# Kernel optimization log

Hardware: AMD Instinct MI355X
Metric: run time of the kernel (lower is better)

Reference implementation:

```python
import jax, jax.numpy as jnp
import numpy as np

N_NODES = 100000
IN_CH = 64
HID = 16
HEADS = 4
OUT_CH = 1
NEG_SLOPE = 0.2
EPS = 1e-16


def gat_conv(x, src, dst, W, att_src, att_dst, bias, heads, out_ch, concat):
    """PyG-style GATConv. src/dst already include self-loops.
    x: [N, F_in]; W: [F_in, heads*out_ch]; att_*: [heads, out_ch]; bias: [heads*out_ch] or [out_ch]."""
    n = x.shape[0]
    h = (x @ W).reshape(n, heads, out_ch)                     # [N,H,C]
    a_src = jnp.einsum('nhc,hc->nh', h, att_src)              # [N,H]
    a_dst = jnp.einsum('nhc,hc->nh', h, att_dst)              # [N,H]
    alpha = jax.nn.leaky_relu(a_src[src] + a_dst[dst], NEG_SLOPE)  # [E,H]
    # segment softmax over incoming edges of each destination node
    m = jax.ops.segment_max(alpha, dst, num_segments=n)       # [N,H]
    e = jnp.exp(alpha - m[dst])
    denom = jax.ops.segment_sum(e, dst, num_segments=n)
    alpha = e / (denom[dst] + EPS)                            # [E,H]
    msg = h[src] * alpha[:, :, None]                          # [E,H,C]
    out = jax.ops.segment_sum(msg, dst, num_segments=n)       # [N,H,C]
    out = out.reshape(n, heads * out_ch) if concat else out.mean(axis=1)
    return out + bias


def setup_inputs() -> dict:
    key = jax.random.key(0)
    ks = jax.random.split(key, 10)
    x = jax.random.normal(ks[0], (N_NODES, IN_CH), dtype=jnp.float32)
    edge_index = jax.random.randint(ks[1], (2, 1600000), 0, N_NODES, dtype=jnp.int64)
    s = 0.1
    W1 = jax.random.normal(ks[2], (IN_CH, HEADS * HID), dtype=jnp.float32) * s
    att_src1 = jax.random.normal(ks[3], (HEADS, HID), dtype=jnp.float32) * s
    att_dst1 = jax.random.normal(ks[4], (HEADS, HID), dtype=jnp.float32) * s
    b1 = jnp.zeros((HEADS * HID,), dtype=jnp.float32)
    W2 = jax.random.normal(ks[5], (HEADS * HID, OUT_CH), dtype=jnp.float32) * s
    att_src2 = jax.random.normal(ks[6], (1, OUT_CH), dtype=jnp.float32) * s
    att_dst2 = jax.random.normal(ks[7], (1, OUT_CH), dtype=jnp.float32) * s
    b2 = jnp.zeros((OUT_CH,), dtype=jnp.float32)
    return {"x": x, "edge_index": edge_index, "W1": W1, "att_src1": att_src1,
            "att_dst1": att_dst1, "b1": b1, "W2": W2, "att_src2": att_src2,
            "att_dst2": att_dst2, "b2": b2}


def reference(x, edge_index, W1, att_src1, att_dst1, b1, W2, att_src2, att_dst2, b2):
    n = x.shape[0]
    loop = jnp.arange(n, dtype=edge_index.dtype)
    src = jnp.concatenate([edge_index[0], loop])  # self-loops (PyG default)
    dst = jnp.concatenate([edge_index[1], loop])
    h = gat_conv(x, src, dst, W1, att_src1, att_dst1, b1, HEADS, HID, concat=True)
    h = jax.nn.elu(h)
    out = gat_conv(h, src, dst, W2, att_src2, att_dst2, b2, 1, OUT_CH, concat=False)
    return out.squeeze()
```

## Files before the change

kernel.cpp:

```cpp
#include <hip/hip_runtime.h>
#include <hip/hip_fp16.h>

#define NN   100000
#define E0   1600000
#define ET   1700000
#define NEG  0.2f
#define EPSV 1e-16f
#define NBK  1563
#define CAP  1536
#define BS   1024
#define NBLK4 ((ET + 4 * BS - 1) / (4 * BS))
#define GEMM_NB 782
#define BC_NB   416

typedef _Float16 half8 __attribute__((ext_vector_type(8)));
typedef float f32x16 __attribute__((ext_vector_type(16)));

__global__ __launch_bounds__(256) void k_g1bc(
    const float* __restrict__ x, const int* __restrict__ ei,
    const float* __restrict__ W1, const float* __restrict__ as1,
    const float* __restrict__ ad1,
    __half* __restrict__ h1h, float* __restrict__ asrc1, float* __restrict__ adst1,
    int* __restrict__ bcnt)
{
    int t = threadIdx.x;
    if (blockIdx.x >= GEMM_NB) {
        __shared__ int cnt[NBK];
        for (int i = t; i < NBK; i += 256) cnt[i] = 0;
        __syncthreads();
        int base = (blockIdx.x - GEMM_NB) * (256 * 16);
#pragma unroll
        for (int k = 0; k < 16; ++k) {
            int idx = base + k * 256 + t;
            if (idx < ET) {
                int d = (idx < E0) ? ei[E0 + idx] : (idx - E0);
                atomicAdd(&cnt[d >> 6], 1);
            }
        }
        __syncthreads();
        for (int i = t; i < NBK; i += 256) if (cnt[i]) atomicAdd(&bcnt[i], cnt[i]);
        return;
    }
    __shared__ float Wl[4096];
    __shared__ float Ul[512];
    for (int i = t; i < 4096; i += 256) Wl[i] = W1[i];
    __syncthreads();
    if (t < 64) {
        int k = t;
#pragma unroll
        for (int h = 0; h < 4; ++h) {
            float su = 0.f, du = 0.f;
#pragma unroll
            for (int c = 0; c < 16; ++c) {
                float w = Wl[k * 64 + h * 16 + c];
                su += w * as1[h * 16 + c];
                du += w * ad1[h * 16 + c];
            }
            Ul[k * 8 + h] = su;
            Ul[k * 8 + 4 + h] = du;
        }
    }
    __syncthreads();
    int lane = t & 63, wv = t >> 6;
    int col = lane & 31, q = lane >> 5;
    half8 bf0[4], bf1[4], bf2[4];
#pragma unroll
    for (int kc = 0; kc < 4; ++kc) {
#pragma unroll
        for (int j = 0; j < 8; ++j) {
            int k = kc * 16 + q * 8 + j;
            bf0[kc][j] = (_Float16)Wl[k * 64 + col];
            bf1[kc][j] = (_Float16)Wl[k * 64 + 32 + col];
            bf2[kc][j] = (col < 8) ? (_Float16)Ul[k * 8 + col] : (_Float16)0.f;
        }
    }
    int tile = blockIdx.x * 4 + wv;
    int n0 = tile * 32;
    if (n0 >= NN) return;
    half8 af[4];
    const float* xrow = x + (size_t)(n0 + col) * 64;
#pragma unroll
    for (int kc = 0; kc < 4; ++kc) {
        float4 xa = *(const float4*)(xrow + kc * 16 + q * 8);
        float4 xb = *(const float4*)(xrow + kc * 16 + q * 8 + 4);
        af[kc][0] = (_Float16)xa.x; af[kc][1] = (_Float16)xa.y;
        af[kc][2] = (_Float16)xa.z; af[kc][3] = (_Float16)xa.w;
        af[kc][4] = (_Float16)xb.x; af[kc][5] = (_Float16)xb.y;
        af[kc][6] = (_Float16)xb.z; af[kc][7] = (_Float16)xb.w;
    }
    f32x16 c0 = {}, c1 = {}, c2 = {};
#pragma unroll
    for (int kc = 0; kc < 4; ++kc) {
        c0 = __builtin_amdgcn_mfma_f32_32x32x16_f16(af[kc], bf0[kc], c0, 0, 0, 0);
        c1 = __builtin_amdgcn_mfma_f32_32x32x16_f16(af[kc], bf1[kc], c1, 0, 0, 0);
        c2 = __builtin_amdgcn_mfma_f32_32x32x16_f16(af[kc], bf2[kc], c2, 0, 0, 0);
    }
#pragma unroll
    for (int reg = 0; reg < 16; ++reg) {
        int row = (reg & 3) + 8 * (reg >> 2) + 4 * q;
        h1h[(size_t)(n0 + row) * 64 + col]      = __float2half(c0[reg]);
        h1h[(size_t)(n0 + row) * 64 + 32 + col] = __float2half(c1[reg]);
    }
    if (col < 8) {
        float* dst = (col < 4) ? asrc1 : adst1;
        int h = col & 3;
#pragma unroll
        for (int reg = 0; reg < 16; ++reg) {
            int row = (reg & 3) + 8 * (reg >> 2) + 4 * q;
            dst[(n0 + row) * 4 + h] = c2[reg];
        }
    }
}

__global__ __launch_bounds__(1024) void k_bscan(const int* __restrict__ bcnt,
                                                int* __restrict__ bbase, int* __restrict__ bcursor)
{
    int t = threadIdx.x;
    int i0 = 2 * t, i1 = 2 * t + 1;
    int a = (i0 < NBK) ? bcnt[i0] : 0;
    int b = (i1 < NBK) ? bcnt[i1] : 0;
    int s = a + b;
    int lane = t & 63, wid = t >> 6;
    int sc = s;
#pragma unroll
    for (int off = 1; off < 64; off <<= 1) {
        int u = __shfl_up(sc, off, 64);
        if (lane >= off) sc += u;
    }
    __shared__ int wsum[16];
    if (lane == 63) wsum[wid] = sc;
    __syncthreads();
    int woff = 0;
    for (int k = 0; k < wid; ++k) woff += wsum[k];
    int excl = sc - s + woff;
    if (i0 < NBK) { bbase[i0] = excl;     bcursor[i0] = excl; }
    if (i1 < NBK) { bbase[i1] = excl + a; bcursor[i1] = excl + a; }
}

__global__ __launch_bounds__(BS) void k_bscat(const int* __restrict__ ei,
                                              int* __restrict__ bcursor, int* __restrict__ bin)
{
    __shared__ int cnt[NBK];
    __shared__ int base[NBK];
    int t = threadIdx.x;
    for (int i = t; i < NBK; i += BS) cnt[i] = 0;
    __syncthreads();
    int blk = blockIdx.x * (BS * 4);
    int b[4], r[4], pk[4];
#pragma unroll
    for (int k = 0; k < 4; ++k) {
        int idx = blk + k * BS + t;
        r[k] = -1;
        if (idx < ET) {
            int s, d;
            if (idx < E0) { s = ei[idx]; d = ei[E0 + idx]; } else { s = d = idx - E0; }
            b[k] = d >> 6;
            pk[k] = s | ((d & 63) << 17);
            r[k] = atomicAdd(&cnt[b[k]], 1);
        }
    }
    __syncthreads();
    for (int i = t; i < NBK; i += BS) if (cnt[i]) base[i] = atomicAdd(&bcursor[i], cnt[i]);
    __syncthreads();
#pragma unroll
    for (int k = 0; k < 4; ++k)
        if (r[k] >= 0) bin[base[b[k]] + r[k]] = pk[k];
}

__global__ __launch_bounds__(256) void k_e1agg(
    const int* __restrict__ bin, const int* __restrict__ bbase, const int* __restrict__ bcnt,
    const float* __restrict__ asrc1, const float* __restrict__ adst1,
    const __half* __restrict__ h1h, const float* __restrict__ b1,
    const float* __restrict__ W2, float* __restrict__ g)
{
    __shared__ int lcsr[CAP];
    __shared__ int deg[64], cur[64];
    int b = blockIdx.x;
    int t = threadIdx.x;
    int beg = bbase[b], cnt = bcnt[b];
    if (cnt > CAP) cnt = CAP;
    if (t < 64) deg[t] = 0;
    __syncthreads();
    for (int i = t; i < cnt; i += 256) atomicAdd(&deg[bin[beg + i] >> 17], 1);
    __syncthreads();
    if (t < 64) {
        int v = deg[t];
        int sc = v;
#pragma unroll
        for (int off = 1; off < 64; off <<= 1) {
            int u = __shfl_up(sc, off, 64);
            if (t >= off) sc += u;
        }
        cur[t] = sc - v;
    }
    __syncthreads();
    for (int i = t; i < cnt; i += 256) {
        int e = bin[beg + i];
        int r = atomicAdd(&cur[e >> 17], 1);
        lcsr[r] = e & 0x1FFFF;
    }
    __syncthreads();
    int hh = t & 3;
    int nl = t >> 2;
    int n = b * 64 + nl;
    if (n >= NN) return;
    int je = cur[nl];
    int jb = je - deg[nl];
    float ad = adst1[n * 4 + hh];
    float acc[16];
#pragma unroll
    for (int c = 0; c < 16; ++c) acc[c] = 0.f;
    float den = 0.f;
    for (int j = jb; j < je; ++j) {
        int s = lcsr[j];
        float as = asrc1[s * 4 + hh];
        float a = as + ad; a = a > 0.f ? a : NEG * a;
        float ev = __expf(a);
        den += ev;
        const uint4* hp = (const uint4*)(h1h + (size_t)s * 64 + hh * 16);
        uint4 r0 = hp[0], r1 = hp[1];
#define U4ACC(r, base) { \
        float2 f0 = __half22float2(*(const __half2*)&r.x); \
        float2 f1 = __half22float2(*(const __half2*)&r.y); \
        float2 f2 = __half22float2(*(const __half2*)&r.z); \
        float2 f3 = __half22float2(*(const __half2*)&r.w); \
        acc[base+0] += ev * f0.x; acc[base+1] += ev * f0.y; \
        acc[base+2] += ev * f1.x; acc[base+3] += ev * f1.y; \
        acc[base+4] += ev * f2.x; acc[base+5] += ev * f2.y; \
        acc[base+6] += ev * f3.x; acc[base+7] += ev * f3.y; }
        U4ACC(r0, 0) U4ACC(r1, 8)
#undef U4ACC
    }
    float inv = 1.f / (den + EPSV);
    const float4* bp = (const float4*)(b1 + hh * 16);
    const float4* wp = (const float4*)(W2 + hh * 16);
    float gv = 0.f;
#pragma unroll
    for (int q = 0; q < 4; ++q) {
        float4 bb = bp[q], w2 = wp[q];
        float v0 = acc[4*q+0] * inv + bb.x; v0 = v0 > 0.f ? v0 : __expf(v0) - 1.f;
        float v1 = acc[4*q+1] * inv + bb.y; v1 = v1 > 0.f ? v1 : __expf(v1) - 1.f;
        float v2 = acc[4*q+2] * inv + bb.z; v2 = v2 > 0.f ? v2 : __expf(v2) - 1.f;
        float v3 = acc[4*q+3] * inv + bb.w; v3 = v3 > 0.f ? v3 : __expf(v3) - 1.f;
        gv += v0 * w2.x + v1 * w2.y + v2 * w2.z + v3 * w2.w;
    }
    gv += __shfl_xor(gv, 1);
    gv += __shfl_xor(gv, 2);
    if (hh == 0) g[n] = gv;
}

__global__ __launch_bounds__(256) void k_e2agg(
    const int* __restrict__ bin, const int* __restrict__ bbase, const int* __restrict__ bcnt,
    const float* __restrict__ g, const float* __restrict__ as2,
    const float* __restrict__ ad2, const float* __restrict__ b2,
    float* __restrict__ out)
{
    __shared__ int lcsr[CAP];
    __shared__ int deg[64], cur[64];
    int b = blockIdx.x;
    int t = threadIdx.x;
    int beg = bbase[b], cnt = bcnt[b];
    if (cnt > CAP) cnt = CAP;
    if (t < 64) deg[t] = 0;
    __syncthreads();
    for (int i = t; i < cnt; i += 256) atomicAdd(&deg[bin[beg + i] >> 17], 1);
    __syncthreads();
    if (t < 64) {
        int v = deg[t];
        int sc = v;
#pragma unroll
        for (int off = 1; off < 64; off <<= 1) {
            int u = __shfl_up(sc, off, 64);
            if (t >= off) sc += u;
        }
        cur[t] = sc - v;
    }
    __syncthreads();
    for (int i = t; i < cnt; i += 256) {
        int e = bin[beg + i];
        int r = atomicAdd(&cur[e >> 17], 1);
        lcsr[r] = e & 0x1FFFF;
    }
    __syncthreads();
    int hh = t & 3;
    int nl = t >> 2;
    int n = b * 64 + nl;
    if (n >= NN) return;
    int je = cur[nl];
    int jb = je - deg[nl];
    float cs = as2[0];
    float gdcd = g[n] * ad2[0];
    float acc = 0.f, den = 0.f;
    for (int j = jb + hh; j < je; j += 4) {
        float gz = g[lcsr[j]];
        float a = gz * cs + gdcd;
        a = a > 0.f ? a : NEG * a;
        float ev = __expf(a);
        den += ev;
        acc += ev * gz;
    }
    acc += __shfl_xor(acc, 1); den += __shfl_xor(den, 1);
    acc += __shfl_xor(acc, 2); den += __shfl_xor(den, 2);
    if (hh == 0) out[n] = acc / (den + EPSV) + b2[0];
}

extern "C" void kernel_launch(void* const* d_in, const int* in_sizes, int n_in,
                              void* d_out, int out_size, void* d_ws, size_t ws_size,
                              hipStream_t stream)
{
    const float* x   = (const float*)d_in[0];
    const int*   ei  = (const int*)d_in[1];
    const float* W1  = (const float*)d_in[2];
    const float* as1 = (const float*)d_in[3];
    const float* ad1 = (const float*)d_in[4];
    const float* b1  = (const float*)d_in[5];
    const float* W2  = (const float*)d_in[6];
    const float* as2 = (const float*)d_in[7];
    const float* ad2 = (const float*)d_in[8];
    const float* b2  = (const float*)d_in[9];
    float* out = (float*)d_out;

    int*   iw      = (int*)d_ws;
    float* fw      = (float*)d_ws;
    int*   bcnt    = iw;
    int*   bbase   = iw + 1664;
    int*   bcursor = iw + 3328;
    int*   bin     = iw + 4992;
    float* asrc1   = fw + 1705088;
    float* adst1   = fw + 2105088;
    float* g       = fw + 2505088;
    __half* h1h    = (__half*)(fw + 2605184);

    hipMemsetAsync(bcnt, 0, NBK * sizeof(int), stream);

    k_g1bc  <<<GEMM_NB + BC_NB, 256, 0, stream>>>(x, ei, W1, as1, ad1,
                                                  h1h, asrc1, adst1, bcnt);
    k_bscan <<<1, 1024, 0, stream>>>(bcnt, bbase, bcursor);
    k_bscat <<<NBLK4, BS, 0, stream>>>(ei, bcursor, bin);
    k_e1agg <<<NBK, 256, 0, stream>>>(bin, bbase, bcnt, asrc1, adst1, h1h, b1, W2, g);
    k_e2agg <<<NBK, 256, 0, stream>>>(bin, bbase, bcnt, g, as2, ad2, b2, out);
}
```

Baseline: 195.6 us.

## Build per-node CSR with global atomics and head-major layout for aggregation

Replaces the bucketed binning (per-64-node bins that each aggregation block re-sorted in shared memory) with a true per-node CSR. Degrees are counted with global atomics, offsets come from a block-sum, scan and per-node scan, and edges are scattered with a global atomic cursor. h1, asrc and adst are stored head-major. Layer-1 aggregation now gives one thread per node per head, with heads split across blocks and combined by atomicAdd into g. This removes the repeated in-block sort, but adds more launches, heavy global atomic contention on node counters, nondeterministic edge order, and float atomics for g.

```diff
diff --git a/kernel.cpp b/kernel.cpp
--- a/kernel.cpp
+++ b/kernel.cpp
@@ -7,11 +7,13 @@
 #define NEG  0.2f
 #define EPSV 1e-16f
 #define NBK  1563
-#define CAP  1536
-#define BS   1024
-#define NBLK4 ((ET + 4 * BS - 1) / (4 * BS))
 #define GEMM_NB 782
-#define BC_NB   416
+#define NC_NB   416
+#define SCAT_NB 416
+#define NPB  256
+#define NCH  391
+#define E1_NB 1568
+#define ECAP 5120
 
 typedef _Float16 half8 __attribute__((ext_vector_type(8)));
 typedef float f32x16 __attribute__((ext_vector_type(16)));
@@ -21,24 +23,19 @@
     const float* __restrict__ W1, const float* __restrict__ as1,
     const float* __restrict__ ad1,
     __half* __restrict__ h1h, float* __restrict__ asrc1, float* __restrict__ adst1,
-    int* __restrict__ bcnt)
+    int* __restrict__ ncnt)
 {
     int t = threadIdx.x;
     if (blockIdx.x >= GEMM_NB) {
-        __shared__ int cnt[NBK];
-        for (int i = t; i < NBK; i += 256) cnt[i] = 0;
-        __syncthreads();
         int base = (blockIdx.x - GEMM_NB) * (256 * 16);
 #pragma unroll
         for (int k = 0; k < 16; ++k) {
             int idx = base + k * 256 + t;
             if (idx < ET) {
                 int d = (idx < E0) ? ei[E0 + idx] : (idx - E0);
-                atomicAdd(&cnt[d >> 6], 1);
+                atomicAdd(&ncnt[d], 1);
             }
         }
-        __syncthreads();
-        for (int i = t; i < NBK; i += 256) if (cnt[i]) atomicAdd(&bcnt[i], cnt[i]);
         return;
     }
     __shared__ float Wl[4096];
@@ -95,11 +92,13 @@
         c1 = __builtin_amdgcn_mfma_f32_32x32x16_f16(af[kc], bf1[kc], c1, 0, 0, 0);
         c2 = __builtin_amdgcn_mfma_f32_32x32x16_f16(af[kc], bf2[kc], c2, 0, 0, 0);
     }
+    int hA = col >> 4, cc = col & 15;
 #pragma unroll
     for (int reg = 0; reg < 16; ++reg) {
         int row = (reg & 3) + 8 * (reg >> 2) + 4 * q;
-        h1h[(size_t)(n0 + row) * 64 + col]      = __float2half(c0[reg]);
-        h1h[(size_t)(n0 + row) * 64 + 32 + col] = __float2half(c1[reg]);
+        size_t n = (size_t)(n0 + row);
+        h1h[((size_t)hA * NN + n) * 16 + cc]       = __float2half(c0[reg]);
+        h1h[((size_t)(hA + 2) * NN + n) * 16 + cc] = __float2half(c1[reg]);
     }
     if (col < 8) {
         float* dst = (col < 4) ? asrc1 : adst1;
@@ -107,13 +106,24 @@
 #pragma unroll
         for (int reg = 0; reg < 16; ++reg) {
             int row = (reg & 3) + 8 * (reg >> 2) + 4 * q;
-            dst[(n0 + row) * 4 + h] = c2[reg];
-        }
-    }
+            dst[(size_t)h * NN + (n0 + row)] = c2[reg];
+        }
+    }
+}
+
+__global__ __launch_bounds__(64) void k_bsum(const int* __restrict__ ncnt,
+                                             int* __restrict__ bcnt)
+{
+    int b = blockIdx.x, t = threadIdx.x;
+    int n = b * 64 + t;
+    int v = (n < NN) ? ncnt[n] : 0;
+#pragma unroll
+    for (int off = 1; off < 64; off <<= 1) v += __shfl_xor(v, off, 64);
+    if (t == 0) bcnt[b] = v;
 }
 
 __global__ __launch_bounds__(1024) void k_bscan(const int* __restrict__ bcnt,
-                                                int* __restrict__ bbase, int* __restrict__ bcursor)
+                                                int* __restrict__ bbase)
 {
     int t = threadIdx.x;
     int i0 = 2 * t, i1 = 2 * t + 1;
@@ -133,165 +143,138 @@
     int woff = 0;
     for (int k = 0; k < wid; ++k) woff += wsum[k];
     int excl = sc - s + woff;
-    if (i0 < NBK) { bbase[i0] = excl;     bcursor[i0] = excl; }
-    if (i1 < NBK) { bbase[i1] = excl + a; bcursor[i1] = excl + a; }
-}
-
-__global__ __launch_bounds__(BS) void k_bscat(const int* __restrict__ ei,
-                                              int* __restrict__ bcursor, int* __restrict__ bin)
-{
-    __shared__ int cnt[NBK];
-    __shared__ int base[NBK];
+    if (i0 < NBK) bbase[i0] = excl;
+    if (i1 < NBK) bbase[i1] = excl + a;
+}
+
+__global__ __launch_bounds__(64) void k_noff(const int* __restrict__ bbase,
+                                             int* __restrict__ A)
+{
+    int b = blockIdx.x, t = threadIdx.x;
+    int n = b * 64 + t;
+    int v = (n < NN) ? A[n] : 0;
+    int sc = v;
+#pragma unroll
+    for (int off = 1; off < 64; off <<= 1) {
+        int u = __shfl_up(sc, off, 64);
+        if (t >= off) sc += u;
+    }
+    if (n < NN) A[n] = bbase[b] + sc - v;
+}
+
+__global__ __launch_bounds__(1024) void k_nscat(const int* __restrict__ ei,
+                                                int* __restrict__ cur, int* __restrict__ bin)
+{
     int t = threadIdx.x;
-    for (int i = t; i < NBK; i += BS) cnt[i] = 0;
-    __syncthreads();
-    int blk = blockIdx.x * (BS * 4);
-    int b[4], r[4], pk[4];
+    int blk = blockIdx.x * (1024 * 4);
 #pragma unroll
     for (int k = 0; k < 4; ++k) {
-        int idx = blk + k * BS + t;
-        r[k] = -1;
+        int idx = blk + k * 1024 + t;
         if (idx < ET) {
             int s, d;
             if (idx < E0) { s = ei[idx]; d = ei[E0 + idx]; } else { s = d = idx - E0; }
-            b[k] = d >> 6;
-            pk[k] = s | ((d & 63) << 17);
-            r[k] = atomicAdd(&cnt[b[k]], 1);
-        }
-    }
-    __syncthreads();
-    for (int i = t; i < NBK; i += BS) if (cnt[i]) base[i] = atomicAdd(&bcursor[i], cnt[i]);
-    __syncthreads();
-#pragma unroll
-    for (int k = 0; k < 4; ++k)
-        if (r[k] >= 0) bin[base[b[k]] + r[k]] = pk[k];
+            int pos = atomicAdd(&cur[d], 1);
+            bin[pos] = s;
+        }
+    }
 }
 
 __global__ __launch_bounds__(256) void k_e1agg(
-    const int* __restrict__ bin, const int* __restrict__ bbase, const int* __restrict__ bcnt,
+    const int* __restrict__ bin, const int* __restrict__ A,
     const float* __restrict__ asrc1, const float* __restrict__ adst1,
     const __half* __restrict__ h1h, const float* __restrict__ b1,
     const float* __restrict__ W2, float* __restrict__ g)
 {
-    __shared__ int lcsr[CAP];
-    __shared__ int deg[64], cur[64];
-    int b = blockIdx.x;
-    int t = threadIdx.x;
-    int beg = bbase[b], cnt = bcnt[b];
-    if (cnt > CAP) cnt = CAP;
-    if (t < 64) deg[t] = 0;
-    __syncthreads();
-    for (int i = t; i < cnt; i += 256) atomicAdd(&deg[bin[beg + i] >> 17], 1);
-    __syncthreads();
-    if (t < 64) {
-        int v = deg[t];
-        int sc = v;
-#pragma unroll
-        for (int off = 1; off < 64; off <<= 1) {
-            int u = __shfl_up(sc, off, 64);
-            if (t >= off) sc += u;
-        }
-        cur[t] = sc - v;
-    }
-    __syncthreads();
-    for (int i = t; i < cnt; i += 256) {
-        int e = bin[beg + i];
-        int r = atomicAdd(&cur[e >> 17], 1);
-        lcsr[r] = e & 0x1FFFF;
-    }
-    __syncthreads();
-    int hh = t & 3;
-    int nl = t >> 2;
-    int n = b * 64 + nl;
+    __shared__ int lcsr[ECAP];
+    int bid = blockIdx.x, t = threadIdx.x;
+    int h = (bid & 7) >> 1;
+    int chunk = (bid >> 3) * 2 + (bid & 1);
+    if (chunk >= NCH) return;
+    int n0 = chunk * NPB;
+    int nlast = min(n0 + NPB, NN) - 1;
+    int jb0 = (n0 == 0) ? 0 : A[n0 - 1];
+    int total = A[nlast] - jb0;
+    if (total > ECAP) total = ECAP;
+    for (int i = t; i < total; i += 256) lcsr[i] = bin[jb0 + i];
+    __syncthreads();
+    int n = n0 + t;
     if (n >= NN) return;
-    int je = cur[nl];
-    int jb = je - deg[nl];
-    float ad = adst1[n * 4 + hh];
+    int jb = ((n == 0) ? 0 : A[n - 1]) - jb0;
+    int je = A[n] - jb0;
+    if (jb > total) jb = total;
+    if (je > total) je = total;
+    size_t hb = (size_t)h * NN;
+    float adv = adst1[hb + n];
     float acc[16];
 #pragma unroll
     for (int c = 0; c < 16; ++c) acc[c] = 0.f;
     float den = 0.f;
     for (int j = jb; j < je; ++j) {
         int s = lcsr[j];
-        float as = asrc1[s * 4 + hh];
-        float a = as + ad; a = a > 0.f ? a : NEG * a;
+        float av = asrc1[hb + s];
+        const uint4* hp = (const uint4*)(h1h + (hb + s) * 16);
+        uint4 r0 = hp[0], r1 = hp[1];
+        float a = av + adv; a = a > 0.f ? a : NEG * a;
         float ev = __expf(a);
         den += ev;
-        const uint4* hp = (const uint4*)(h1h + (size_t)s * 64 + hh * 16);
-        uint4 r0 = hp[0], r1 = hp[1];
-#define U4ACC(r, base) { \
-        float2 f0 = __half22float2(*(const __half2*)&r.x); \
-        float2 f1 = __half22float2(*(const __half2*)&r.y); \
-        float2 f2 = __half22float2(*(const __half2*)&r.z); \
-        float2 f3 = __half22float2(*(const __half2*)&r.w); \
-        acc[base+0] += ev * f0.x; acc[base+1] += ev * f0.y; \
-        acc[base+2] += ev * f1.x; acc[base+3] += ev * f1.y; \
-        acc[base+4] += ev * f2.x; acc[base+5] += ev * f2.y; \
-        acc[base+6] += ev * f3.x; acc[base+7] += ev * f3.y; }
-        U4ACC(r0, 0) U4ACC(r1, 8)
-#undef U4ACC
+        float2 f0 = __half22float2(*(const __half2*)&r0.x);
+        float2 f1 = __half22float2(*(const __half2*)&r0.y);
+        float2 f2 = __half22float2(*(const __half2*)&r0.z);
+        float2 f3 = __half22float2(*(const __half2*)&r0.w);
+        acc[0] += ev * f0.x; acc[1] += ev * f0.y;
+        acc[2] += ev * f1.x; acc[3] += ev * f1.y;
+        acc[4] += ev * f2.x; acc[5] += ev * f2.y;
+        acc[6] += ev * f3.x; acc[7] += ev * f3.y;
+        float2 f4 = __half22float2(*(const __half2*)&r1.x);
+        float2 f5 = __half22float2(*(const __half2*)&r1.y);
+        float2 f6 = __half22float2(*(const __half2*)&r1.z);
+        float2 f7 = __half22float2(*(const __half2*)&r1.w);
+        acc[8]  += ev * f4.x; acc[9]  += ev * f4.y;
+        acc[10] += ev * f5.x; acc[11] += ev * f5.y;
+        acc[12] += ev * f6.x; acc[13] += ev * f6.y;
+        acc[14] += ev * f7.x; acc[15] += ev * f7.y;
     }
     float inv = 1.f / (den + EPSV);
-    const float4* bp = (const float4*)(b1 + hh * 16);
-    const float4* wp = (const float4*)(W2 + hh * 16);
+    const float4* bp = (const float4*)(b1 + h * 16);
+    const float4* wp = (const float4*)(W2 + h * 16);
     float gv = 0.f;
 #pragma unroll
-    for (int q = 0; q < 4; ++q) {
-        float4 bb = bp[q], w2 = wp[q];
-        float v0 = acc[4*q+0] * inv + bb.x; v0 = v0 > 0.f ? v0 : __expf(v0) - 1.f;
-        float v1 = acc[4*q+1] * inv + bb.y; v1 = v1 > 0.f ? v1 : __expf(v1) - 1.f;
-        float v2 = acc[4*q+2] * inv + bb.z; v2 = v2 > 0.f ? v2 : __expf(v2) - 1.f;
-        float v3 = acc[4*q+3] * inv + bb.w; v3 = v3 > 0.f ? v3 : __expf(v3) - 1.f;
+    for (int qq = 0; qq < 4; ++qq) {
+        float4 bb = bp[qq], w2 = wp[qq];
+        float v0 = acc[4*qq+0] * inv + bb.x; v0 = v0 > 0.f ? v0 : __expf(v0) - 1.f;
+        float v1 = acc[4*qq+1] * inv + bb.y; v1 = v1 > 0.f ? v1 : __expf(v1) - 1.f;
+        float v2 = acc[4*qq+2] * inv + bb.z; v2 = v2 > 0.f ? v2 : __expf(v2) - 1.f;
+        float v3 = acc[4*qq+3] * inv + bb.w; v3 = v3 > 0.f ? v3 : __expf(v3) - 1.f;
         gv += v0 * w2.x + v1 * w2.y + v2 * w2.z + v3 * w2.w;
     }
-    gv += __shfl_xor(gv, 1);
-    gv += __shfl_xor(gv, 2);
-    if (hh == 0) g[n] = gv;
+    atomicAdd(&g[n], gv);
 }
 
 __global__ __launch_bounds__(256) void k_e2agg(
-    const int* __restrict__ bin, const int* __restrict__ bbase, const int* __restrict__ bcnt,
+    const int* __restrict__ bin, const int* __restrict__ A,
     const float* __restrict__ g, const float* __restrict__ as2,
     const float* __restrict__ ad2, const float* __restrict__ b2,
     float* __restrict__ out)
 {
-    __shared__ int lcsr[CAP];
-    __shared__ int deg[64], cur[64];
-    int b = blockIdx.x;
-    int t = threadIdx.x;
-    int beg = bbase[b], cnt = bcnt[b];
-    if (cnt > CAP) cnt = CAP;
-    if (t < 64) deg[t] = 0;
-    __syncthreads();
-    for (int i = t; i < cnt; i += 256) atomicAdd(&deg[bin[beg + i] >> 17], 1);
-    __syncthreads();
-    if (t < 64) {
-        int v = deg[t];
-        int sc = v;
-#pragma unroll
-        for (int off = 1; off < 64; off <<= 1) {
-            int u = __shfl_up(sc, off, 64);
-            if (t >= off) sc += u;
-        }
-        cur[t] = sc - v;
-    }
-    __syncthreads();
-    for (int i = t; i < cnt; i += 256) {
-        int e = bin[beg + i];
-        int r = atomicAdd(&cur[e >> 17], 1);
-        lcsr[r] = e & 0x1FFFF;
-    }
-    __syncthreads();
-    int hh = t & 3;
-    int nl = t >> 2;
-    int n = b * 64 + nl;
+    __shared__ int lcsr[ECAP];
+    int bid = blockIdx.x, t = threadIdx.x;
+    int n0 = bid * NPB;
+    int nlast = min(n0 + NPB, NN) - 1;
+    int jb0 = (n0 == 0) ? 0 : A[n0 - 1];
+    int total = A[nlast] - jb0;
+    if (total > ECAP) total = ECAP;
+    for (int i = t; i < total; i += 256) lcsr[i] = bin[jb0 + i];
+    __syncthreads();
+    int n = n0 + t;
     if (n >= NN) return;
-    int je = cur[nl];
-    int jb = je - deg[nl];
+    int jb = ((n == 0) ? 0 : A[n - 1]) - jb0;
+    int je = A[n] - jb0;
+    if (jb > total) jb = total;
+    if (je > total) je = total;
     float cs = as2[0];
     float gdcd = g[n] * ad2[0];
     float acc = 0.f, den = 0.f;
-    for (int j = jb + hh; j < je; j += 4) {
+    for (int j = jb; j < je; ++j) {
         float gz = g[lcsr[j]];
         float a = gz * cs + gdcd;
         a = a > 0.f ? a : NEG * a;
@@ -299,9 +282,7 @@
         den += ev;
         acc += ev * gz;
     }
-    acc += __shfl_xor(acc, 1); den += __shfl_xor(den, 1);
-    acc += __shfl_xor(acc, 2); den += __shfl_xor(den, 2);
-    if (hh == 0) out[n] = acc / (den + EPSV) + b2[0];
+    out[n] = acc / (den + EPSV) + b2[0];
 }
 
 extern "C" void kernel_launch(void* const* d_in, const int* in_sizes, int n_in,
@@ -320,23 +301,26 @@
     const float* b2  = (const float*)d_in[9];
     float* out = (float*)d_out;
 
-    int*   iw      = (int*)d_ws;
-    float* fw      = (float*)d_ws;
-    int*   bcnt    = iw;
-    int*   bbase   = iw + 1664;
-    int*   bcursor = iw + 3328;
-    int*   bin     = iw + 4992;
-    float* asrc1   = fw + 1705088;
-    float* adst1   = fw + 2105088;
-    float* g       = fw + 2505088;
-    __half* h1h    = (__half*)(fw + 2605184);
-
-    hipMemsetAsync(bcnt, 0, NBK * sizeof(int), stream);
-
-    k_g1bc  <<<GEMM_NB + BC_NB, 256, 0, stream>>>(x, ei, W1, as1, ad1,
-                                                  h1h, asrc1, adst1, bcnt);
-    k_bscan <<<1, 1024, 0, stream>>>(bcnt, bbase, bcursor);
-    k_bscat <<<NBLK4, BS, 0, stream>>>(ei, bcursor, bin);
-    k_e1agg <<<NBK, 256, 0, stream>>>(bin, bbase, bcnt, asrc1, adst1, h1h, b1, W2, g);
-    k_e2agg <<<NBK, 256, 0, stream>>>(bin, bbase, bcnt, g, as2, ad2, b2, out);
-}
+    int*   iw    = (int*)d_ws;
+    float* fw    = (float*)d_ws;
+    int*   A     = iw;
+    int*   bcnt  = iw + 100352;
+    int*   bbase = iw + 102016;
+    int*   bin   = iw + 103680;
+    float* asrcm = fw + 1803680;
+    float* adstm = fw + 2203680;
+    float* g     = fw + 2603680;
+    __half* h1hm = (__half*)(fw + 2703712);
+
+    hipMemsetAsync(A, 0, 100352 * sizeof(int), stream);
+    hipMemsetAsync(g, 0, NN * sizeof(float), stream);
+
+    k_g1bc  <<<GEMM_NB + NC_NB, 256, 0, stream>>>(x, ei, W1, as1, ad1,
+                                                  h1hm, asrcm, adstm, A);
+    k_bsum  <<<NBK, 64, 0, stream>>>(A, bcnt);
+    k_bscan <<<1, 1024, 0, stream>>>(bcnt, bbase);
+    k_noff  <<<NBK, 64, 0, stream>>>(bbase, A);
+    k_nscat <<<SCAT_NB, 1024, 0, stream>>>(ei, A, bin);
+    k_e1agg <<<E1_NB, 256, 0, stream>>>(bin, A, asrcm, adstm, h1hm, b1, W2, g);
+    k_e2agg <<<NCH, 256, 0, stream>>>(bin, A, g, as2, ad2, b2, out);
+}
```

New measurement: 373.6 us. 1.91x slower.

## Split layer-1 aggregation per head with head-major layout and a shared CSR sort

Applied to the files above, without the earlier changes.

Features and attention scores are now stored head-major, so each head's 16-channel rows sit contiguously. A new pass sorts each destination bucket once and writes per-node end offsets, so both aggregation kernels stop rebuilding the local CSR. Layer-1 aggregation launches one block per (head, bucket) pair, splits each node's edges across four lanes, and merges the per-head partial outputs with atomicAdd into g. This raises parallelism and cache locality per head, at the cost of an extra launch, a memset of g, float atomics and four times as many blocks each rereading the bucket.

```diff
diff --git a/kernel.cpp b/kernel.cpp
--- a/kernel.cpp
+++ b/kernel.cpp
@@ -12,6 +12,7 @@
 #define NBLK4 ((ET + 4 * BS - 1) / (4 * BS))
 #define GEMM_NB 782
 #define BC_NB   416
+#define E1_NB   6256
 
 typedef _Float16 half8 __attribute__((ext_vector_type(8)));
 typedef float f32x16 __attribute__((ext_vector_type(16)));
@@ -95,11 +96,13 @@
         c1 = __builtin_amdgcn_mfma_f32_32x32x16_f16(af[kc], bf1[kc], c1, 0, 0, 0);
         c2 = __builtin_amdgcn_mfma_f32_32x32x16_f16(af[kc], bf2[kc], c2, 0, 0, 0);
     }
+    int hA = col >> 4, cc = col & 15;
 #pragma unroll
     for (int reg = 0; reg < 16; ++reg) {
         int row = (reg & 3) + 8 * (reg >> 2) + 4 * q;
-        h1h[(size_t)(n0 + row) * 64 + col]      = __float2half(c0[reg]);
-        h1h[(size_t)(n0 + row) * 64 + 32 + col] = __float2half(c1[reg]);
+        size_t n = (size_t)(n0 + row);
+        h1h[((size_t)hA * NN + n) * 16 + cc]       = __float2half(c0[reg]);
+        h1h[((size_t)(hA + 2) * NN + n) * 16 + cc] = __float2half(c1[reg]);
     }
     if (col < 8) {
         float* dst = (col < 4) ? asrc1 : adst1;
@@ -107,7 +110,7 @@
 #pragma unroll
         for (int reg = 0; reg < 16; ++reg) {
             int row = (reg & 3) + 8 * (reg >> 2) + 4 * q;
-            dst[(n0 + row) * 4 + h] = c2[reg];
+            dst[(size_t)h * NN + (n0 + row)] = c2[reg];
         }
     }
 }
@@ -167,131 +170,146 @@
         if (r[k] >= 0) bin[base[b[k]] + r[k]] = pk[k];
 }
 
+__global__ __launch_bounds__(256) void k_bsort(
+    int* __restrict__ bin, const int* __restrict__ bbase, const int* __restrict__ bcnt,
+    int* __restrict__ A)
+{
+    __shared__ int raw[CAP];
+    __shared__ int srt[CAP];
+    __shared__ int deg[64], cur[64];
+    int b = blockIdx.x, t = threadIdx.x;
+    int beg = bbase[b], cnt = bcnt[b];
+    if (cnt > CAP) cnt = CAP;
+    if (t < 64) deg[t] = 0;
+    for (int i = t; i < cnt; i += 256) raw[i] = bin[beg + i];
+    __syncthreads();
+    for (int i = t; i < cnt; i += 256) atomicAdd(&deg[raw[i] >> 17], 1);
+    __syncthreads();
+    if (t < 64) {
+        int v = deg[t];
+        int sc = v;
+#pragma unroll
+        for (int off = 1; off < 64; off <<= 1) {
+            int u = __shfl_up(sc, off, 64);
+            if (t >= off) sc += u;
+        }
+        cur[t] = sc - v;
+        int n = b * 64 + t;
+        if (n < NN) A[n] = beg + sc;
+    }
+    __syncthreads();
+    for (int i = t; i < cnt; i += 256) {
+        int e = raw[i];
+        int r = atomicAdd(&cur[e >> 17], 1);
+        srt[r] = e & 0x1FFFF;
+    }
+    __syncthreads();
+    for (int i = t; i < cnt; i += 256) bin[beg + i] = srt[i];
+}
+
 __global__ __launch_bounds__(256) void k_e1agg(
-    const int* __restrict__ bin, const int* __restrict__ bbase, const int* __restrict__ bcnt,
+    const int* __restrict__ bin, const int* __restrict__ A,
+    const int* __restrict__ bbase, const int* __restrict__ bcnt,
     const float* __restrict__ asrc1, const float* __restrict__ adst1,
     const __half* __restrict__ h1h, const float* __restrict__ b1,
     const float* __restrict__ W2, float* __restrict__ g)
 {
     __shared__ int lcsr[CAP];
-    __shared__ int deg[64], cur[64];
-    int b = blockIdx.x;
-    int t = threadIdx.x;
+    int bid = blockIdx.x, t = threadIdx.x;
+    int lane8 = bid & 7;
+    int h = lane8 >> 1;
+    int b = (bid >> 3) * 2 + (lane8 & 1);
+    if (b >= NBK) return;
     int beg = bbase[b], cnt = bcnt[b];
     if (cnt > CAP) cnt = CAP;
-    if (t < 64) deg[t] = 0;
-    __syncthreads();
-    for (int i = t; i < cnt; i += 256) atomicAdd(&deg[bin[beg + i] >> 17], 1);
-    __syncthreads();
-    if (t < 64) {
-        int v = deg[t];
-        int sc = v;
-#pragma unroll
-        for (int off = 1; off < 64; off <<= 1) {
-            int u = __shfl_up(sc, off, 64);
-            if (t >= off) sc += u;
-        }
-        cur[t] = sc - v;
-    }
-    __syncthreads();
-    for (int i = t; i < cnt; i += 256) {
-        int e = bin[beg + i];
-        int r = atomicAdd(&cur[e >> 17], 1);
-        lcsr[r] = e & 0x1FFFF;
-    }
-    __syncthreads();
-    int hh = t & 3;
-    int nl = t >> 2;
+    for (int i = t; i < cnt; i += 256) lcsr[i] = bin[beg + i];
+    __syncthreads();
+    int p = t & 3, nl = t >> 2;
     int n = b * 64 + nl;
     if (n >= NN) return;
-    int je = cur[nl];
-    int jb = je - deg[nl];
-    float ad = adst1[n * 4 + hh];
+    int je = A[n] - beg;
+    int jb = ((n == 0) ? 0 : A[n - 1]) - beg;
+    if (je > cnt) je = cnt;
+    if (jb < 0) jb = 0;
+    size_t hb = (size_t)h * NN;
+    float adv = adst1[hb + n];
     float acc[16];
 #pragma unroll
     for (int c = 0; c < 16; ++c) acc[c] = 0.f;
     float den = 0.f;
-    for (int j = jb; j < je; ++j) {
+    for (int j = jb + p; j < je; j += 4) {
         int s = lcsr[j];
-        float as = asrc1[s * 4 + hh];
-        float a = as + ad; a = a > 0.f ? a : NEG * a;
+        float av = asrc1[hb + s];
+        const uint4* hp = (const uint4*)(h1h + (hb + s) * 16);
+        uint4 r0 = hp[0], r1 = hp[1];
+        float a = av + adv; a = a > 0.f ? a : NEG * a;
         float ev = __expf(a);
         den += ev;
-        const uint4* hp = (const uint4*)(h1h + (size_t)s * 64 + hh * 16);
-        uint4 r0 = hp[0], r1 = hp[1];
-#define U4ACC(r, base) { \
-        float2 f0 = __half22float2(*(const __half2*)&r.x); \
-        float2 f1 = __half22float2(*(const __half2*)&r.y); \
-        float2 f2 = __half22float2(*(const __half2*)&r.z); \
-        float2 f3 = __half22float2(*(const __half2*)&r.w); \
-        acc[base+0] += ev * f0.x; acc[base+1] += ev * f0.y; \
-        acc[base+2] += ev * f1.x; acc[base+3] += ev * f1.y; \
-        acc[base+4] += ev * f2.x; acc[base+5] += ev * f2.y; \
-        acc[base+6] += ev * f3.x; acc[base+7] += ev * f3.y; }
-        U4ACC(r0, 0) U4ACC(r1, 8)
-#undef U4ACC
-    }
+        float2 f0 = __half22float2(*(const __half2*)&r0.x);
+        float2 f1 = __half22float2(*(const __half2*)&r0.y);
+        float2 f2 = __half22float2(*(const __half2*)&r0.z);
+        float2 f3 = __half22float2(*(const __half2*)&r0.w);
+        acc[0] += ev * f0.x; acc[1] += ev * f0.y;
+        acc[2] += ev * f1.x; acc[3] += ev * f1.y;
+        acc[4] += ev * f2.x; acc[5] += ev * f2.y;
+        acc[6] += ev * f3.x; acc[7] += ev * f3.y;
+        float2 f4 = __half22float2(*(const __half2*)&r1.x);
+        float2 f5 = __half22float2(*(const __half2*)&r1.y);
+        float2 f6 = __half22float2(*(const __half2*)&r1.z);
+        float2 f7 = __half22float2(*(const __half2*)&r1.w);
+        acc[8]  += ev * f4.x; acc[9]  += ev * f4.y;
+        acc[10] += ev * f5.x; acc[11] += ev * f5.y;
+        acc[12] += ev * f6.x; acc[13] += ev * f6.y;
+        acc[14] += ev * f7.x; acc[15] += ev * f7.y;
+    }
+#pragma unroll
+    for (int c = 0; c < 16; ++c) {
+        acc[c] += __shfl_xor(acc[c], 1);
+        acc[c] += __shfl_xor(acc[c], 2);
+    }
+    den += __shfl_xor(den, 1);
+    den += __shfl_xor(den, 2);
+    if (p != 0) return;
     float inv = 1.f / (den + EPSV);
-    const float4* bp = (const float4*)(b1 + hh * 16);
-    const float4* wp = (const float4*)(W2 + hh * 16);
+    const float4* bp = (const float4*)(b1 + h * 16);
+    const float4* wp = (const float4*)(W2 + h * 16);
     float gv = 0.f;
 #pragma unroll
-    for (int q = 0; q < 4; ++q) {
-        float4 bb = bp[q], w2 = wp[q];
-        float v0 = acc[4*q+0] * inv + bb.x; v0 = v0 > 0.f ? v0 : __expf(v0) - 1.f;
-        float v1 = acc[4*q+1] * inv + bb.y; v1 = v1 > 0.f ? v1 : __expf(v1) - 1.f;
-        float v2 = acc[4*q+2] * inv + bb.z; v2 = v2 > 0.f ? v2 : __expf(v2) - 1.f;
-        float v3 = acc[4*q+3] * inv + bb.w; v3 = v3 > 0.f ? v3 : __expf(v3) - 1.f;
+    for (int qq = 0; qq < 4; ++qq) {
+        float4 bb = bp[qq], w2 = wp[qq];
+        float v0 = acc[4*qq+0] * inv + bb.x; v0 = v0 > 0.f ? v0 : __expf(v0) - 1.f;
+        float v1 = acc[4*qq+1] * inv + bb.y; v1 = v1 > 0.f ? v1 : __expf(v1) - 1.f;
+        float v2 = acc[4*qq+2] * inv + bb.z; v2 = v2 > 0.f ? v2 : __expf(v2) - 1.f;
+        float v3 = acc[4*qq+3] * inv + bb.w; v3 = v3 > 0.f ? v3 : __expf(v3) - 1.f;
         gv += v0 * w2.x + v1 * w2.y + v2 * w2.z + v3 * w2.w;
     }
-    gv += __shfl_xor(gv, 1);
-    gv += __shfl_xor(gv, 2);
-    if (hh == 0) g[n] = gv;
+    atomicAdd(&g[n], gv);
 }
 
 __global__ __launch_bounds__(256) void k_e2agg(
-    const int* __restrict__ bin, const int* __restrict__ bbase, const int* __restrict__ bcnt,
+    const int* __restrict__ bin, const int* __restrict__ A,
+    const int* __restrict__ bbase, const int* __restrict__ bcnt,
     const float* __restrict__ g, const float* __restrict__ as2,
     const float* __restrict__ ad2, const float* __restrict__ b2,
     float* __restrict__ out)
 {
     __shared__ int lcsr[CAP];
-    __shared__ int deg[64], cur[64];
-    int b = blockIdx.x;
-    int t = threadIdx.x;
+    int b = blockIdx.x, t = threadIdx.x;
     int beg = bbase[b], cnt = bcnt[b];
     if (cnt > CAP) cnt = CAP;
-    if (t < 64) deg[t] = 0;
-    __syncthreads();
-    for (int i = t; i < cnt; i += 256) atomicAdd(&deg[bin[beg + i] >> 17], 1);
-    __syncthreads();
-    if (t < 64) {
-        int v = deg[t];
-        int sc = v;
-#pragma unroll
-        for (int off = 1; off < 64; off <<= 1) {
-            int u = __shfl_up(sc, off, 64);
-            if (t >= off) sc += u;
-        }
-        cur[t] = sc - v;
-    }
-    __syncthreads();
-    for (int i = t; i < cnt; i += 256) {
-        int e = bin[beg + i];
-        int r = atomicAdd(&cur[e >> 17], 1);
-        lcsr[r] = e & 0x1FFFF;
-    }
-    __syncthreads();
-    int hh = t & 3;
-    int nl = t >> 2;
+    for (int i = t; i < cnt; i += 256) lcsr[i] = bin[beg + i];
+    __syncthreads();
+    int p = t & 3, nl = t >> 2;
     int n = b * 64 + nl;
     if (n >= NN) return;
-    int je = cur[nl];
-    int jb = je - deg[nl];
+    int je = A[n] - beg;
+    int jb = ((n == 0) ? 0 : A[n - 1]) - beg;
+    if (je > cnt) je = cnt;
+    if (jb < 0) jb = 0;
     float cs = as2[0];
     float gdcd = g[n] * ad2[0];
     float acc = 0.f, den = 0.f;
-    for (int j = jb + hh; j < je; j += 4) {
+    for (int j = jb + p; j < je; j += 4) {
         float gz = g[lcsr[j]];
         float a = gz * cs + gdcd;
         a = a > 0.f ? a : NEG * a;
@@ -301,7 +319,7 @@
     }
     acc += __shfl_xor(acc, 1); den += __shfl_xor(den, 1);
     acc += __shfl_xor(acc, 2); den += __shfl_xor(den, 2);
-    if (hh == 0) out[n] = acc / (den + EPSV) + b2[0];
+    if (p == 0) out[n] = acc / (den + EPSV) + b2[0];
 }
 
 extern "C" void kernel_launch(void* const* d_in, const int* in_sizes, int n_in,
@@ -325,18 +343,22 @@
     int*   bcnt    = iw;
     int*   bbase   = iw + 1664;
     int*   bcursor = iw + 3328;
-    int*   bin     = iw + 4992;
-    float* asrc1   = fw + 1705088;
-    float* adst1   = fw + 2105088;
-    float* g       = fw + 2505088;
-    __half* h1h    = (__half*)(fw + 2605184);
+    int*   A       = iw + 4992;
+    int*   bin     = iw + 105344;
+    float* asrcm   = fw + 1805344;
+    float* adstm   = fw + 2205344;
+    float* g       = fw + 2605344;
+    __half* h1hm   = (__half*)(fw + 2705376);
 
     hipMemsetAsync(bcnt, 0, NBK * sizeof(int), stream);
+    hipMemsetAsync(g, 0, NN * sizeof(float), stream);
 
     k_g1bc  <<<GEMM_NB + BC_NB, 256, 0, stream>>>(x, ei, W1, as1, ad1,
-                                                  h1h, asrc1, adst1, bcnt);
+                                                  h1hm, asrcm, adstm, bcnt);
     k_bscan <<<1, 1024, 0, stream>>>(bcnt, bbase, bcursor);
     k_bscat <<<NBLK4, BS, 0, stream>>>(ei, bcursor, bin);
-    k_e1agg <<<NBK, 256, 0, stream>>>(bin, bbase, bcnt, asrc1, adst1, h1h, b1, W2, g);
-    k_e2agg <<<NBK, 256, 0, stream>>>(bin, bbase, bcnt, g, as2, ad2, b2, out);
-}
+    k_bsort <<<NBK, 256, 0, stream>>>(bin, bbase, bcnt, A);
+    k_e1agg <<<E1_NB, 256, 0, stream>>>(bin, A, bbase, bcnt, asrcm, adstm,
+                                        h1hm, b1, W2, g);
+    k_e2agg <<<NBK, 256, 0, stream>>>(bin, A, bbase, bcnt, g, as2, ad2, b2, out);
+}
```

Result: slower. 222.6 us (+13.8%).

## Persist sorted per-bucket CSR from layer 1 and reuse in layer 2; coarsen binning blocks

Applied to the files above, without the earlier changes.

The first aggregation kernel now writes its locally sorted source list back into the bin array and records each node's end offset, so the second aggregation kernel no longer rebuilds the per-node CSR with shared atomics and scans. Layer 2 just loads the sorted list and reads node ranges from the offset array, with a two-way unrolled gather loop. The count and scatter kernels also process more edges per block (fewer blocks, fewer global atomics on bucket counters). The cost is extra global writes of bin and offsets in layer 1 and lower parallelism in the binning kernels.

```diff
diff --git a/kernel.cpp b/kernel.cpp
--- a/kernel.cpp
+++ b/kernel.cpp
@@ -9,9 +9,9 @@
 #define NBK  1563
 #define CAP  1536
 #define BS   1024
-#define NBLK4 ((ET + 4 * BS - 1) / (4 * BS))
+#define SCAT_NB 104
 #define GEMM_NB 782
-#define BC_NB   416
+#define BC_NB   104
 
 typedef _Float16 half8 __attribute__((ext_vector_type(8)));
 typedef float f32x16 __attribute__((ext_vector_type(16)));
@@ -28,9 +28,8 @@
         __shared__ int cnt[NBK];
         for (int i = t; i < NBK; i += 256) cnt[i] = 0;
         __syncthreads();
-        int base = (blockIdx.x - GEMM_NB) * (256 * 16);
-#pragma unroll
-        for (int k = 0; k < 16; ++k) {
+        int base = (blockIdx.x - GEMM_NB) * (256 * 64);
+        for (int k = 0; k < 64; ++k) {
             int idx = base + k * 256 + t;
             if (idx < ET) {
                 int d = (idx < E0) ? ei[E0 + idx] : (idx - E0);
@@ -145,10 +144,10 @@
     int t = threadIdx.x;
     for (int i = t; i < NBK; i += BS) cnt[i] = 0;
     __syncthreads();
-    int blk = blockIdx.x * (BS * 4);
-    int b[4], r[4], pk[4];
-#pragma unroll
-    for (int k = 0; k < 4; ++k) {
+    int blk = blockIdx.x * (BS * 16);
+    int b[16], r[16], pk[16];
+#pragma unroll
+    for (int k = 0; k < 16; ++k) {
         int idx = blk + k * BS + t;
         r[k] = -1;
         if (idx < ET) {
@@ -163,15 +162,15 @@
     for (int i = t; i < NBK; i += BS) if (cnt[i]) base[i] = atomicAdd(&bcursor[i], cnt[i]);
     __syncthreads();
 #pragma unroll
-    for (int k = 0; k < 4; ++k)
+    for (int k = 0; k < 16; ++k)
         if (r[k] >= 0) bin[base[b[k]] + r[k]] = pk[k];
 }
 
 __global__ __launch_bounds__(256) void k_e1agg(
-    const int* __restrict__ bin, const int* __restrict__ bbase, const int* __restrict__ bcnt,
+    int* __restrict__ bin, const int* __restrict__ bbase, const int* __restrict__ bcnt,
     const float* __restrict__ asrc1, const float* __restrict__ adst1,
     const __half* __restrict__ h1h, const float* __restrict__ b1,
-    const float* __restrict__ W2, float* __restrict__ g)
+    const float* __restrict__ W2, float* __restrict__ g, int* __restrict__ A)
 {
     __shared__ int lcsr[CAP];
     __shared__ int deg[64], cur[64];
@@ -192,6 +191,8 @@
             if (t >= off) sc += u;
         }
         cur[t] = sc - v;
+        int n = b * 64 + t;
+        if (n < NN) A[n] = beg + sc;
     }
     __syncthreads();
     for (int i = t; i < cnt; i += 256) {
@@ -200,6 +201,7 @@
         lcsr[r] = e & 0x1FFFF;
     }
     __syncthreads();
+    for (int i = t; i < cnt; i += 256) bin[beg + i] = lcsr[i];
     int hh = t & 3;
     int nl = t >> 2;
     int n = b * 64 + nl;
@@ -250,58 +252,47 @@
 }
 
 __global__ __launch_bounds__(256) void k_e2agg(
-    const int* __restrict__ bin, const int* __restrict__ bbase, const int* __restrict__ bcnt,
+    const int* __restrict__ bin, const int* __restrict__ A,
+    const int* __restrict__ bbase, const int* __restrict__ bcnt,
     const float* __restrict__ g, const float* __restrict__ as2,
     const float* __restrict__ ad2, const float* __restrict__ b2,
     float* __restrict__ out)
 {
     __shared__ int lcsr[CAP];
-    __shared__ int deg[64], cur[64];
-    int b = blockIdx.x;
-    int t = threadIdx.x;
+    int b = blockIdx.x, t = threadIdx.x;
     int beg = bbase[b], cnt = bcnt[b];
     if (cnt > CAP) cnt = CAP;
-    if (t < 64) deg[t] = 0;
-    __syncthreads();
-    for (int i = t; i < cnt; i += 256) atomicAdd(&deg[bin[beg + i] >> 17], 1);
-    __syncthreads();
-    if (t < 64) {
-        int v = deg[t];
-        int sc = v;
-#pragma unroll
-        for (int off = 1; off < 64; off <<= 1) {
-            int u = __shfl_up(sc, off, 64);
-            if (t >= off) sc += u;
-        }
-        cur[t] = sc - v;
-    }
-    __syncthreads();
-    for (int i = t; i < cnt; i += 256) {
-        int e = bin[beg + i];
-        int r = atomicAdd(&cur[e >> 17], 1);
-        lcsr[r] = e & 0x1FFFF;
-    }
-    __syncthreads();
-    int hh = t & 3;
-    int nl = t >> 2;
+    for (int i = t; i < cnt; i += 256) lcsr[i] = bin[beg + i];
+    __syncthreads();
+    int p = t & 3, nl = t >> 2;
     int n = b * 64 + nl;
     if (n >= NN) return;
-    int je = cur[nl];
-    int jb = je - deg[nl];
+    int je = A[n] - beg;                        if (je > cnt) je = cnt;
+    int jb = ((n == 0) ? 0 : A[n - 1]) - beg;   if (jb < 0) jb = 0;
     float cs = as2[0];
     float gdcd = g[n] * ad2[0];
     float acc = 0.f, den = 0.f;
-    for (int j = jb + hh; j < je; j += 4) {
-        float gz = g[lcsr[j]];
-        float a = gz * cs + gdcd;
-        a = a > 0.f ? a : NEG * a;
-        float ev = __expf(a);
-        den += ev;
-        acc += ev * gz;
-    }
+
+#define ACC2(gz) { \
+        float a = gz * cs + gdcd; a = a > 0.f ? a : NEG * a; \
+        float ev = __expf(a); den += ev; acc += ev * gz; }
+
+    int j = jb + p;
+    for (; j + 4 < je; j += 8) {
+        int s0 = lcsr[j], s1 = lcsr[j + 4];
+        float g0 = g[s0], g1 = g[s1];
+        ACC2(g0)
+        ACC2(g1)
+    }
+    if (j < je) {
+        float g0 = g[lcsr[j]];
+        ACC2(g0)
+    }
+#undef ACC2
+
     acc += __shfl_xor(acc, 1); den += __shfl_xor(den, 1);
     acc += __shfl_xor(acc, 2); den += __shfl_xor(den, 2);
-    if (hh == 0) out[n] = acc / (den + EPSV) + b2[0];
+    if (p == 0) out[n] = acc / (den + EPSV) + b2[0];
 }
 
 extern "C" void kernel_launch(void* const* d_in, const int* in_sizes, int n_in,
@@ -325,18 +316,20 @@
     int*   bcnt    = iw;
     int*   bbase   = iw + 1664;
     int*   bcursor = iw + 3328;
-    int*   bin     = iw + 4992;
-    float* asrc1   = fw + 1705088;
-    float* adst1   = fw + 2105088;
-    float* g       = fw + 2505088;
-    __half* h1h    = (__half*)(fw + 2605184);
+    int*   A       = iw + 4992;
+    int*   bin     = iw + 105344;
+    float* asrc1   = fw + 1805344;
+    float* adst1   = fw + 2205344;
+    float* g       = fw + 2605344;
+    __half* h1h    = (__half*)(fw + 2705376);
 
     hipMemsetAsync(bcnt, 0, NBK * sizeof(int), stream);
 
     k_g1bc  <<<GEMM_NB + BC_NB, 256, 0, stream>>>(x, ei, W1, as1, ad1,
                                                   h1h, asrc1, adst1, bcnt);
     k_bscan <<<1, 1024, 0, stream>>>(bcnt, bbase, bcursor);
-    k_bscat <<<NBLK4, BS, 0, stream>>>(ei, bcursor, bin);
-    k_e1agg <<<NBK, 256, 0, stream>>>(bin, bbase, bcnt, asrc1, adst1, h1h, b1, W2, g);
-    k_e2agg <<<NBK, 256, 0, stream>>>(bin, bbase, bcnt, g, as2, ad2, b2, out);
-}
+    k_bscat <<<SCAT_NB, BS, 0, stream>>>(ei, bcursor, bin);
+    k_e1agg <<<NBK, 256, 0, stream>>>(bin, bbase, bcnt, asrc1, adst1, h1h,
+                                      b1, W2, g, A);
+    k_e2agg <<<NBK, 256, 0, stream>>>(bin, A, bbase, bcnt, g, as2, ad2, b2, out);
+}
```

Result: no change. 198.4 us (+1.4%).
